# Optimization experiments

Measured on AMD Instinct MI355X. Metric: run time of the kernel, lower is better.

## Reference

```python
import jax, jax.numpy as jnp
import numpy as np
import math

B, S, E = 2, 2048, 1024
H, HD = 16, 64  # num_heads, head_size


def setup_inputs() -> dict:
    key = jax.random.key(0)
    ks = jax.random.split(key, 9)
    sc = 1.0 / math.sqrt(HD)
    return {
        "x": jax.random.normal(ks[0], (B, S, E), dtype=jnp.float32),
        "Wq_w": jax.random.normal(ks[1], (HD, HD), dtype=jnp.float32) * sc,
        "Wq_b": jax.random.normal(ks[2], (HD,), dtype=jnp.float32) * 0.02,
        "Wk_w": jax.random.normal(ks[3], (HD, HD), dtype=jnp.float32) * sc,
        "Wk_b": jax.random.normal(ks[4], (HD,), dtype=jnp.float32) * 0.02,
        "Wv_w": jax.random.normal(ks[5], (HD, HD), dtype=jnp.float32) * sc,
        "Wv_b": jax.random.normal(ks[6], (HD,), dtype=jnp.float32) * 0.02,
        "proj_w": jax.random.normal(ks[7], (E, E), dtype=jnp.float32) * (1.0 / math.sqrt(E)),
        "proj_b": jax.random.normal(ks[8], (E,), dtype=jnp.float32) * 0.02,
    }


def reference(x, Wq_w, Wq_b, Wk_w, Wk_b, Wv_w, Wv_b, proj_w, proj_b):
    b, s, _ = x.shape
    xh = x.reshape(b, s, H, HD)  # split heads; QKV linears act per-head (shared weights)
    # torch Linear: y = x @ W.T + b
    q = jnp.einsum('bshd,ed->bhse', xh, Wq_w) + Wq_b  # [B,H,S,HD]
    k = jnp.einsum('bshd,ed->bhse', xh, Wk_w) + Wk_b
    v = jnp.einsum('bshd,ed->bhse', xh, Wv_w) + Wv_b
    scores = jnp.einsum('bhqd,bhkd->bhqk', q, k) / math.sqrt(HD)
    causal = jnp.tril(jnp.ones((s, s), dtype=bool))
    scores = jnp.where(causal, scores, jnp.float32(-1e20))
    attn = jax.nn.softmax(scores, axis=-1)  # attn_dropout p=0 (eval)
    out = jnp.einsum('bhqk,bhkd->bqhd', attn, v).reshape(b, s, H * HD)
    out = out @ proj_w.T + proj_b  # resid_dropout p=0 (eval)
    return out
```

## Files before the change

kernel.cpp:

```cpp
#include <hip/hip_runtime.h>
#include <hip/hip_bf16.h>

#define B_ 2
#define S_ 2048
#define E_ 1024
#define H_ 16
#define HD_ 64
#define T_ (B_ * S_)

typedef short bf16x8 __attribute__((ext_vector_type(8)));
typedef short bf16x4 __attribute__((ext_vector_type(4)));
typedef float f32x4 __attribute__((ext_vector_type(4)));

__device__ __forceinline__ short f2bf(float f) {
  union { float f; unsigned u; } v;
  v.f = f;
  unsigned r = v.u + 0x7fffu + ((v.u >> 16) & 1u);
  return (short)(r >> 16);
}


__global__ __launch_bounds__(256) void qkv_conv_kernel(
    const float* __restrict__ x,
    const float* __restrict__ wq, const float* __restrict__ bq,
    const float* __restrict__ wk, const float* __restrict__ bk,
    const float* __restrict__ wv, const float* __restrict__ bv,
    short* __restrict__ Q, short* __restrict__ KV,
    const float* __restrict__ pw, short* __restrict__ pwb) {
  const int tid = threadIdx.x;
  if (blockIdx.x >= 512) {
    int i = ((blockIdx.x - 512) * 256 + tid) * 4;
    float4 f = *(const float4*)(pw + i);
    bf16x4 o;
    o[0] = f2bf(f.x); o[1] = f2bf(f.y); o[2] = f2bf(f.z); o[3] = f2bf(f.w);
    *(bf16x4*)(pwb + i) = o;
    return;
  }
  __shared__ short Xs[64][136];
  __shared__ short Ws[192][72];
  __shared__ short Qt[64][68], Kt[64][68], Vt[64][68];

  const int bid = blockIdx.x;
  const int tb = bid >> 3, hg = bid & 7;
  const int s0 = (tb * 64) & (S_ - 1);
  const int kt = s0 >> 6;
  const int bb = (tb * 64) >> 11;
  const int wave = tid >> 6, lane = tid & 63;
  const int lrow = lane & 15, quad = lane >> 4;

#pragma unroll
  for (int i = 0; i < 8; i++) {
    int c = tid + 256 * i;
    int row = c >> 5, col4 = c & 31;
    float4 f = *(const float4*)(x + ((long)(tb * 64 + row)) * E_ + hg * 128 + col4 * 4);
    bf16x4 o;
    o[0] = f2bf(f.x); o[1] = f2bf(f.y); o[2] = f2bf(f.z); o[3] = f2bf(f.w);
    *(bf16x4*)&Xs[row][col4 * 4] = o;
  }
#pragma unroll
  for (int m = 0; m < 3; m++) {
    const float* w = (m == 0) ? wq : (m == 1) ? wk : wv;
#pragma unroll
    for (int i = 0; i < 4; i++) {
      int c = tid + 256 * i;
      int row = m * 64 + (c >> 4), col = (c & 15) * 4;
      float4 f = *(const float4*)(w + (long)c * 4);
      bf16x4 o;
      o[0] = f2bf(f.x); o[1] = f2bf(f.y); o[2] = f2bf(f.z); o[3] = f2bf(f.w);
      *(bf16x4*)&Ws[row][col] = o;
    }
  }
  float bias[12];
#pragma unroll
  for (int nb = 0; nb < 12; nb++) {
    int sel = nb >> 2;
    int e = ((nb & 3) * 16) + lrow;
    bias[nb] = ((sel == 0) ? bq : (sel == 1) ? bk : bv)[e];
  }
  __syncthreads();

  bf16x8 bf0[12], bf1[12];
#pragma unroll
  for (int nb = 0; nb < 12; nb++) {
    bf0[nb] = *(bf16x8*)&Ws[nb * 16 + lrow][quad * 8];
    bf1[nb] = *(bf16x8*)&Ws[nb * 16 + lrow][32 + quad * 8];
  }

  const float QSCALE = 0.125f * 1.44269504089f;
  for (int hl = 0; hl < 2; hl++) {
    const int h = hg * 2 + hl;
    bf16x8 a0 = *(bf16x8*)&Xs[wave * 16 + lrow][hl * 64 + quad * 8];
    bf16x8 a1 = *(bf16x8*)&Xs[wave * 16 + lrow][hl * 64 + 32 + quad * 8];
#pragma unroll
    for (int nb = 0; nb < 12; nb++) {
      f32x4 acc = {0.f, 0.f, 0.f, 0.f};
      acc = __builtin_amdgcn_mfma_f32_16x16x32_bf16(a0, bf0[nb], acc, 0, 0, 0);
      acc = __builtin_amdgcn_mfma_f32_16x16x32_bf16(a1, bf1[nb], acc, 0, 0, 0);
      const int sel = nb >> 2;
      const float scale = (sel == 0) ? QSCALE : 1.0f;
      short (*ct)[68] = (sel == 0) ? Qt : (sel == 1) ? Kt : Vt;
#pragma unroll
      for (int r = 0; r < 4; r++) {
        ct[wave * 16 + quad * 4 + r][(nb & 3) * 16 + lrow] =
            f2bf((acc[r] + bias[nb]) * scale);
      }
    }
    __syncthreads();

    const int bh = bb * H_ + h;
    short* Qg = Q + ((long)bh * S_ + s0) * HD_;
    short* Tg = KV + ((long)(bh * 32 + kt)) * 8192;
#pragma unroll
    for (int i = 0; i < 2; i++) {
      int c = tid + 256 * i;
      int row = c >> 3, col = (c & 7) * 8;
      *(bf16x8*)(Qg + (long)row * HD_ + col) = *(bf16x8*)&Qt[row][col];
    }
#pragma unroll
    for (int u = 0; u < 4; u++) {
      int fid = tid + 256 * u;
      bf16x8 val;
      int lane2 = fid & 63;
      int quad2 = lane2 >> 4, lrow2 = lane2 & 15;
      if (u < 2) {
        int g = fid >> 6;
        int nb = g >> 1, half = g & 1;
        val = *(bf16x8*)&Kt[nb * 16 + lrow2][half * 32 + quad2 * 8];
      } else {
        int g = (fid >> 6) & 7;
        int p2 = g >> 2, db = g & 3;
#pragma unroll
        for (int j = 0; j < 8; j++) {
          int key = (2 * p2 + (j >> 2)) * 16 + quad2 * 4 + (j & 3);
          val[j] = Vt[key][db * 16 + lrow2];
        }
      }
      *(bf16x8*)(Tg + fid * 8) = val;
    }
    __syncthreads();
  }
}

__global__ __launch_bounds__(256) void attn_kernel(
    const short* __restrict__ Q, const short* __restrict__ KV,
    short* __restrict__ O ) {
  const int tid = threadIdx.x;
  const int bid = blockIdx.x;
  const int bh = bid & 31;
  const int g = 31 - (bid >> 5);
  const int b = bh >> 4, h = bh & 15;
  const long qbase = ((long)bh) << 17;

  const int wave = tid >> 6, lane = tid & 63;
  const int lrow = lane & 15, quad = lane >> 4;
  const int qs = 4 * g + wave;
  const int qg = qs * 16 + lrow;

  const short* qp = Q + qbase + (long)qg * HD_;
  bf16x8 qf0 = *(const bf16x8*)(qp + quad * 8);
  bf16x8 qf1 = *(const bf16x8*)(qp + 32 + quad * 8);

  const short* tb = KV + ((long)bh * 32) * 8192 + lane * 8;

  f32x4 Oacc[4];
#pragma unroll
  for (int db = 0; db < 4; db++) Oacc[db] = f32x4{0.f, 0.f, 0.f, 0.f};
  float lsum = 0.f;

  const int nkt = g + 1;
  for (int kt = 0; kt < nkt; kt++) {
    const short* tp = tb + (long)kt * 8192;

    bf16x8 kf[8];
#pragma unroll
    for (int g2 = 0; g2 < 8; g2++) kf[g2] = *(const bf16x8*)(tp + g2 * 512);

    f32x4 sc[4];
#pragma unroll
    for (int nb = 0; nb < 4; nb++) {
      f32x4 acc = {0.f, 0.f, 0.f, 0.f};
      acc = __builtin_amdgcn_mfma_f32_16x16x32_bf16(kf[2 * nb], qf0, acc, 0, 0, 0);
      acc = __builtin_amdgcn_mfma_f32_16x16x32_bf16(kf[2 * nb + 1], qf1, acc, 0, 0, 0);
      sc[nb] = acc;
    }

    bf16x8 vf[8];
#pragma unroll
    for (int g2 = 0; g2 < 8; g2++) vf[g2] = *(const bf16x8*)(tp + 4096 + g2 * 512);

    if (kt == nkt - 1) {
      const int k0 = kt * 64;
#pragma unroll
      for (int nb = 0; nb < 4; nb++) {
        int kgl = k0 + nb * 16 + quad * 4;
#pragma unroll
        for (int r = 0; r < 4; r++)
          if (kgl + r > qg) sc[nb][r] = -1e30f;
      }
    }

    bf16x4 pf[4];
#pragma unroll
    for (int nb = 0; nb < 4; nb++) {
      unsigned u[4];
#pragma unroll
      for (int r = 0; r < 4; r++) {
        float p = __builtin_amdgcn_exp2f(sc[nb][r]);
        lsum += p;
        u[r] = __float_as_uint(p) + 0x8000u;
      }
      unsigned lo = __builtin_amdgcn_perm(u[1], u[0], 0x07060302u);
      unsigned hi = __builtin_amdgcn_perm(u[3], u[2], 0x07060302u);
      union { unsigned q[2]; bf16x4 v; } pk;
      pk.q[0] = lo; pk.q[1] = hi;
      pf[nb] = pk.v;
    }

#pragma unroll
    for (int p2 = 0; p2 < 2; p2++) {
#pragma unroll
      for (int db = 0; db < 4; db++) {
        bf16x8 vv = vf[p2 * 4 + db];
        bf16x4 vlo = {vv[0], vv[1], vv[2], vv[3]};
        bf16x4 vhi = {vv[4], vv[5], vv[6], vv[7]};
        Oacc[db] = __builtin_amdgcn_mfma_f32_16x16x16bf16_1k(vlo, pf[2 * p2], Oacc[db], 0, 0, 0);
        Oacc[db] = __builtin_amdgcn_mfma_f32_16x16x16bf16_1k(vhi, pf[2 * p2 + 1], Oacc[db], 0, 0, 0);
      }
    }
  }

  lsum += __shfl_xor(lsum, 16);
  lsum += __shfl_xor(lsum, 32);
  const float invl = 1.f / lsum;
  const long token = (long)b * S_ + qg;
  short* obase = O + token * E_ + h * HD_;
#pragma unroll
  for (int db = 0; db < 4; db++) {
    bf16x4 o;
#pragma unroll
    for (int r = 0; r < 4; r++) o[r] = f2bf(Oacc[db][r] * invl);
    *(bf16x4*)(obase + db * 16 + quad * 4) = o;
  }
}

__global__ __launch_bounds__(256) void proj_kernel(
    const short* __restrict__ A, const short* __restrict__ W,
    const float* __restrict__ bias, float* __restrict__ out) {
  __shared__ short As[2][128][40];
  __shared__ short Bs[2][64][40];
  const int tid = threadIdx.x;
  const int bid = blockIdx.x;
  const int m0 = (bid >> 4) * 128;
  const int n0 = (bid & 15) * 64;
  const int wave = tid >> 6, lane = tid & 63;
  const int wm = wave >> 1, wn = wave & 1;
  const int lrow = lane & 15, quad = lane >> 4;

  const int ar = tid >> 1, ac = (tid & 1) * 16;
  const int br = tid >> 2, bc = (tid & 3) * 8;

  bf16x8 a0, a1, b0;
  auto LDR = [&](int k0) {
    const short* ap = A + (long)(m0 + ar) * E_ + k0 + ac;
    a0 = *(const bf16x8*)(ap);
    a1 = *(const bf16x8*)(ap + 8);
    b0 = *(const bf16x8*)(W + (long)(n0 + br) * E_ + k0 + bc);
  };

  f32x4 acc[4][2];
#pragma unroll
  for (int i = 0; i < 4; i++)
#pragma unroll
    for (int j = 0; j < 2; j++) acc[i][j] = f32x4{0.f, 0.f, 0.f, 0.f};

  LDR(0);
  for (int kk = 0; kk < 32; kk++) {
    const int buf = kk & 1;
    *(bf16x8*)&As[buf][ar][ac] = a0;
    *(bf16x8*)&As[buf][ar][ac + 8] = a1;
    *(bf16x8*)&Bs[buf][br][bc] = b0;
    __syncthreads();
    if (kk < 31) LDR((kk + 1) * 32);

    bf16x8 af[4], bfr[2];
#pragma unroll
    for (int i = 0; i < 4; i++)
      af[i] = *(bf16x8*)&As[buf][wm * 64 + i * 16 + lrow][quad * 8];
#pragma unroll
    for (int j = 0; j < 2; j++)
      bfr[j] = *(bf16x8*)&Bs[buf][wn * 32 + j * 16 + lrow][quad * 8];
#pragma unroll
    for (int i = 0; i < 4; i++)
#pragma unroll
      for (int j = 0; j < 2; j++)
        acc[i][j] = __builtin_amdgcn_mfma_f32_16x16x32_bf16(af[i], bfr[j], acc[i][j], 0, 0, 0);
  }

#pragma unroll
  for (int j = 0; j < 2; j++) {
    int col = n0 + wn * 32 + j * 16 + lrow;
    float bv = bias[col];
#pragma unroll
    for (int i = 0; i < 4; i++) {
#pragma unroll
      for (int r = 0; r < 4; r++) {
        int row = m0 + wm * 64 + i * 16 + quad * 4 + r;
        out[(long)row * E_ + col] = acc[i][j][r] + bv;
      }
    }
  }
}

extern "C" void kernel_launch(void* const* d_in, const int* in_sizes, int n_in,
                              void* d_out, int out_size, void* d_ws, size_t ws_size,
                              hipStream_t stream) {
  const float* x  = (const float*)d_in[0];
  const float* wq = (const float*)d_in[1];
  const float* bq = (const float*)d_in[2];
  const float* wk = (const float*)d_in[3];
  const float* bk = (const float*)d_in[4];
  const float* wv = (const float*)d_in[5];
  const float* bv = (const float*)d_in[6];
  const float* pw = (const float*)d_in[7];
  const float* pb = (const float*)d_in[8];
  float* out = (float*)d_out;

  char* ws = (char*)d_ws;
  short* Qb = (short*)(ws);
  short* KVb = (short*)(ws + (size_t)8 * 1024 * 1024);
  short* AO = (short*)(ws + (size_t)24 * 1024 * 1024);
  short* PW = (short*)(ws + (size_t)32 * 1024 * 1024);

  qkv_conv_kernel<<<dim3(512 + 1024), dim3(256), 0, stream>>>(
      x, wq, bq, wk, bk, wv, bv, Qb, KVb, pw, PW);
  attn_kernel<<<dim3(32 * 32), dim3(256), 0, stream>>>(Qb, KVb, AO);
  proj_kernel<<<dim3(32 * 16), dim3(256), 0, stream>>>(AO, PW, pb, out);
}
```

Before: 152.3 us.

## Process two query tiles per wave in attention to reuse K/V fragments

```diff
diff --git a/kernel.cpp b/kernel.cpp
--- a/kernel.cpp
+++ b/kernel.cpp
@@ -141,7 +141,7 @@
   }
 }
 
-__global__ __launch_bounds__(256) void attn_kernel(
+__global__ __launch_bounds__(128) void attn_kernel(
     const short* __restrict__ Q, const short* __restrict__ KV,
     short* __restrict__ O ) {
   const int tid = threadIdx.x;
@@ -153,21 +153,28 @@
 
   const int wave = tid >> 6, lane = tid & 63;
   const int lrow = lane & 15, quad = lane >> 4;
-  const int qs = 4 * g + wave;
-  const int qg = qs * 16 + lrow;
-
-  const short* qp = Q + qbase + (long)qg * HD_;
-  bf16x8 qf0 = *(const bf16x8*)(qp + quad * 8);
-  bf16x8 qf1 = *(const bf16x8*)(qp + 32 + quad * 8);
+  const int r0 = g * 64 + wave * 32;
+  const int qgA = r0 + lrow;
+  const int qgB = r0 + 16 + lrow;
+
+  const short* qpA = Q + qbase + (long)qgA * HD_;
+  const short* qpB = Q + qbase + (long)qgB * HD_;
+  bf16x8 qfA0 = *(const bf16x8*)(qpA + quad * 8);
+  bf16x8 qfA1 = *(const bf16x8*)(qpA + 32 + quad * 8);
+  bf16x8 qfB0 = *(const bf16x8*)(qpB + quad * 8);
+  bf16x8 qfB1 = *(const bf16x8*)(qpB + 32 + quad * 8);
 
   const short* tb = KV + ((long)bh * 32) * 8192 + lane * 8;
 
-  f32x4 Oacc[4];
-#pragma unroll
-  for (int db = 0; db < 4; db++) Oacc[db] = f32x4{0.f, 0.f, 0.f, 0.f};
-  float lsum = 0.f;
-
-  const int nkt = g + 1;
+  f32x4 OA[4], OB[4];
+#pragma unroll
+  for (int db = 0; db < 4; db++) {
+    OA[db] = f32x4{0.f, 0.f, 0.f, 0.f};
+    OB[db] = f32x4{0.f, 0.f, 0.f, 0.f};
+  }
+  float lsA = 0.f, lsB = 0.f;
+
+  const int nkt = (r0 + 95) >> 6;
   for (int kt = 0; kt < nkt; kt++) {
     const short* tp = tb + (long)kt * 8192;
 
@@ -175,13 +182,17 @@
 #pragma unroll
     for (int g2 = 0; g2 < 8; g2++) kf[g2] = *(const bf16x8*)(tp + g2 * 512);
 
-    f32x4 sc[4];
+    f32x4 scA[4], scB[4];
 #pragma unroll
     for (int nb = 0; nb < 4; nb++) {
-      f32x4 acc = {0.f, 0.f, 0.f, 0.f};
-      acc = __builtin_amdgcn_mfma_f32_16x16x32_bf16(kf[2 * nb], qf0, acc, 0, 0, 0);
-      acc = __builtin_amdgcn_mfma_f32_16x16x32_bf16(kf[2 * nb + 1], qf1, acc, 0, 0, 0);
-      sc[nb] = acc;
+      f32x4 a = {0.f, 0.f, 0.f, 0.f};
+      a = __builtin_amdgcn_mfma_f32_16x16x32_bf16(kf[2 * nb], qfA0, a, 0, 0, 0);
+      a = __builtin_amdgcn_mfma_f32_16x16x32_bf16(kf[2 * nb + 1], qfA1, a, 0, 0, 0);
+      scA[nb] = a;
+      f32x4 c = {0.f, 0.f, 0.f, 0.f};
+      c = __builtin_amdgcn_mfma_f32_16x16x32_bf16(kf[2 * nb], qfB0, c, 0, 0, 0);
+      c = __builtin_amdgcn_mfma_f32_16x16x32_bf16(kf[2 * nb + 1], qfB1, c, 0, 0, 0);
+      scB[nb] = c;
     }
 
     bf16x8 vf[8];
@@ -194,26 +205,32 @@
       for (int nb = 0; nb < 4; nb++) {
         int kgl = k0 + nb * 16 + quad * 4;
 #pragma unroll
-        for (int r = 0; r < 4; r++)
-          if (kgl + r > qg) sc[nb][r] = -1e30f;
-      }
-    }
-
-    bf16x4 pf[4];
+        for (int r = 0; r < 4; r++) {
+          if (kgl + r > qgA) scA[nb][r] = -1e30f;
+          if (kgl + r > qgB) scB[nb][r] = -1e30f;
+        }
+      }
+    }
+
+    bf16x4 pfA[4], pfB[4];
 #pragma unroll
     for (int nb = 0; nb < 4; nb++) {
-      unsigned u[4];
+      unsigned ua[4], ub[4];
 #pragma unroll
       for (int r = 0; r < 4; r++) {
-        float p = __builtin_amdgcn_exp2f(sc[nb][r]);
-        lsum += p;
-        u[r] = __float_as_uint(p) + 0x8000u;
-      }
-      unsigned lo = __builtin_amdgcn_perm(u[1], u[0], 0x07060302u);
-      unsigned hi = __builtin_amdgcn_perm(u[3], u[2], 0x07060302u);
+        float pa = __builtin_amdgcn_exp2f(scA[nb][r]);
+        float pb2 = __builtin_amdgcn_exp2f(scB[nb][r]);
+        lsA += pa; lsB += pb2;
+        ua[r] = __float_as_uint(pa) + 0x8000u;
+        ub[r] = __float_as_uint(pb2) + 0x8000u;
+      }
       union { unsigned q[2]; bf16x4 v; } pk;
-      pk.q[0] = lo; pk.q[1] = hi;
-      pf[nb] = pk.v;
+      pk.q[0] = __builtin_amdgcn_perm(ua[1], ua[0], 0x07060302u);
+      pk.q[1] = __builtin_amdgcn_perm(ua[3], ua[2], 0x07060302u);
+      pfA[nb] = pk.v;
+      pk.q[0] = __builtin_amdgcn_perm(ub[1], ub[0], 0x07060302u);
+      pk.q[1] = __builtin_amdgcn_perm(ub[3], ub[2], 0x07060302u);
+      pfB[nb] = pk.v;
     }
 
 #pragma unroll
@@ -223,23 +240,31 @@
         bf16x8 vv = vf[p2 * 4 + db];
         bf16x4 vlo = {vv[0], vv[1], vv[2], vv[3]};
         bf16x4 vhi = {vv[4], vv[5], vv[6], vv[7]};
-        Oacc[db] = __builtin_amdgcn_mfma_f32_16x16x16bf16_1k(vlo, pf[2 * p2], Oacc[db], 0, 0, 0);
-        Oacc[db] = __builtin_amdgcn_mfma_f32_16x16x16bf16_1k(vhi, pf[2 * p2 + 1], Oacc[db], 0, 0, 0);
-      }
-    }
-  }
-
-  lsum += __shfl_xor(lsum, 16);
-  lsum += __shfl_xor(lsum, 32);
-  const float invl = 1.f / lsum;
-  const long token = (long)b * S_ + qg;
-  short* obase = O + token * E_ + h * HD_;
+        OA[db] = __builtin_amdgcn_mfma_f32_16x16x16bf16_1k(vlo, pfA[2 * p2], OA[db], 0, 0, 0);
+        OA[db] = __builtin_amdgcn_mfma_f32_16x16x16bf16_1k(vhi, pfA[2 * p2 + 1], OA[db], 0, 0, 0);
+        OB[db] = __builtin_amdgcn_mfma_f32_16x16x16bf16_1k(vlo, pfB[2 * p2], OB[db], 0, 0, 0);
+        OB[db] = __builtin_amdgcn_mfma_f32_16x16x16bf16_1k(vhi, pfB[2 * p2 + 1], OB[db], 0, 0, 0);
+      }
+    }
+  }
+
+  lsA += __shfl_xor(lsA, 16);
+  lsA += __shfl_xor(lsA, 32);
+  lsB += __shfl_xor(lsB, 16);
+  lsB += __shfl_xor(lsB, 32);
+  const float invA = 1.f / lsA, invB = 1.f / lsB;
+  short* oA = O + ((long)b * S_ + qgA) * E_ + h * HD_;
+  short* oB = O + ((long)b * S_ + qgB) * E_ + h * HD_;
 #pragma unroll
   for (int db = 0; db < 4; db++) {
-    bf16x4 o;
-#pragma unroll
-    for (int r = 0; r < 4; r++) o[r] = f2bf(Oacc[db][r] * invl);
-    *(bf16x4*)(obase + db * 16 + quad * 4) = o;
+    bf16x4 oa, ob;
+#pragma unroll
+    for (int r = 0; r < 4; r++) {
+      oa[r] = f2bf(OA[db][r] * invA);
+      ob[r] = f2bf(OB[db][r] * invB);
+    }
+    *(bf16x4*)(oA + db * 16 + quad * 4) = oa;
+    *(bf16x4*)(oB + db * 16 + quad * 4) = ob;
   }
 }
 
@@ -333,6 +358,6 @@
 
   qkv_conv_kernel<<<dim3(512 + 1024), dim3(256), 0, stream>>>(
       x, wq, bq, wk, bk, wv, bv, Qb, KVb, pw, PW);
-  attn_kernel<<<dim3(32 * 32), dim3(256), 0, stream>>>(Qb, KVb, AO);
+  attn_kernel<<<dim3(32 * 32), dim3(128), 0, stream>>>(Qb, KVb, AO);
   proj_kernel<<<dim3(32 * 16), dim3(256), 0, stream>>>(AO, PW, pb, out);
 }
```

Result: slower. 159.2 us (+4.6%).
